# Performance work log

Measured on AMD Instinct MI355X. Metric: run time of the kernel, lower is better.

Reference implementation:

```python
import jax, jax.numpy as jnp
import numpy as np

B, L = 2, 160
RD = 128          # residue_dim
AD = 128          # atom_dim
NUM_AT = 37       # atom37
NSC = 34          # side-chain atom slots (37 - 3 backbone)
EPS = 8.0         # radius for eps_8 graph
NOISE = 0.5       # noise added to repeated CA positions
HID = 512         # decoder MLP hidden


def _precomputed_atom37_mask():
    # Stand-in for VALID_ATOM37_MASK [20 residue types, 37 atoms]:
    # backbone N,CA,C,O always present; deterministic pseudo side-chain counts.
    m = np.zeros((20, NUM_AT), np.float32)
    m[:, :4] = 1.0
    for r in range(20):
        nsc = 1 + (r * 7) % 10
        m[r, 4:4 + nsc] = 1.0
    return jnp.asarray(m)


def setup_inputs() -> dict:
    key = jax.random.key(0)
    ks = jax.random.split(key, 8)
    bb_pred = jax.random.normal(ks[0], (B, L, 3, 3), jnp.float32) * 10.0
    scalar_features = jax.random.normal(ks[1], (B, L, RD), jnp.float32)
    aa_pred = jax.random.normal(ks[2], (B, L, 20), jnp.float32)
    mask = jnp.ones((B, L), jnp.float32)
    residue_batch = jnp.repeat(jnp.arange(B, dtype=jnp.int64), L)
    # learned parameters
    atom_emb = jax.random.normal(ks[3], (NUM_AT, AD), jnp.float32) * 0.02
    W1 = jax.random.normal(ks[4], (2 * AD, HID), jnp.float32) / np.sqrt(2.0 * AD)
    b1 = jnp.zeros((HID,), jnp.float32)
    W2 = jax.random.normal(ks[5], (HID, 3), jnp.float32) / np.sqrt(float(HID))
    b2 = jnp.zeros((3,), jnp.float32)
    # pre-sampled position noise (torch.randn_like * noise)
    pos_noise = jax.random.normal(ks[6], (B, L, NSC, 3), jnp.float32) * NOISE
    precomputed_mask = _precomputed_atom37_mask()
    return dict(bb_pred=bb_pred, scalar_features=scalar_features, aa_pred=aa_pred,
                residue_batch=residue_batch, mask=mask, precomputed_mask=precomputed_mask,
                atom_emb=atom_emb, W1=W1, b1=b1, W2=W2, b2=b2, pos_noise=pos_noise)


def reference(bb_pred, scalar_features, aa_pred, residue_batch, mask,
              precomputed_mask, atom_emb, W1, b1, W2, b2, pos_noise):
    # --- generate_atom37_mask ---
    res_types = jnp.argmax(aa_pred, axis=-1)                       # [B,L]
    atom_mask = precomputed_mask[res_types] * mask[..., None]      # [B,L,37]

    # --- ResidueAndAtomEmbedder (dense, validity carried as mask) ---
    atom_type_emb = atom_emb[None, None] * atom_mask[..., None]    # [B,L,37,AD]
    combined = scalar_features[:, :, None, :] + atom_type_emb      # [B,L,37,AD]
    sc_mask = atom_mask[:, :, 3:]                                  # [B,L,34]
    h = combined[:, :, 3:, :] * sc_mask[..., None]                 # [B,L,34,AD]

    # --- reconstruct_edges: CA repeated per side-chain slot + noise ---
    ca = bb_pred[:, :, 1, :] * mask[..., None]                     # [B,L,3]
    pos = ca[:, :, None, :] + pos_noise                            # [B,L,34,3]

    Ns = L * NSC
    x = pos.reshape(B, Ns, 3)
    hf = h.reshape(B, Ns, AD)
    valid = sc_mask.reshape(B, Ns)                                 # batch axis B == residue_batch separation

    # pairwise squared distances [B,Ns,Ns] (eps_8 radius graph, dense masked form)
    x2 = jnp.sum(x * x, axis=-1)
    d2 = x2[:, :, None] + x2[:, None, :] - 2.0 * jnp.einsum('bnd,bmd->bnm', x, x)
    pair_valid = valid[:, :, None] * valid[:, None, :]
    w = jnp.where(d2 < EPS * EPS, jnp.exp(-d2 / (2.0 * EPS * EPS)), 0.0) * pair_valid

    # --- PositionDecoder (EGNN-style layer, self-loops contribute zero rel-pos) ---
    deg = jnp.sum(w, axis=-1, keepdims=True)                       # [B,Ns,1]
    inv = 1.0 / (deg + 1.0)
    agg_pos = (x * deg - jnp.einsum('bnm,bmd->bnd', w, x)) * inv   # sum_j w_ij (x_i - x_j), normalized
    h_agg = jnp.einsum('bnm,bmd->bnd', w, hf) * inv                # [B,Ns,AD]
    z = jnp.concatenate([hf, h_agg], axis=-1)                      # [B,Ns,2*AD]
    gate = jnp.tanh(jax.nn.relu(z @ W1 + b1) @ W2 + b2)            # [B,Ns,3]
    disp = agg_pos * gate * valid[..., None]

    updated_pos = (x + disp).reshape(B, L, NSC, 3)
    return atom_mask, updated_pos
```

## Files before the change

### kernel.cpp

```cpp
#include <hip/hip_runtime.h>
#include <hip/hip_bf16.h>
#include <math.h>

#define BB 2
#define LL 160
#define NSC 34
#define NS (LL * NSC)
#define TOT (BB * NS)
#define AD 128
#define ADX 144
#define HID 512
#define NAT 37
#define KC 8
#define NVP 1792
#define NVT 28
#define NVPT (BB * NVP)
#define PEN 1.0e9f

typedef __attribute__((ext_vector_type(4))) float f32x4;
typedef __attribute__((ext_vector_type(8))) short s16x8;
typedef __attribute__((address_space(1))) const unsigned int gu32;
typedef __attribute__((address_space(3))) unsigned int lu32;

struct LdsW { float t[64][65]; };
struct LdsPC {
  int sincl[256];
  int smap[NVP];
  short srt[LL];
  float smk[LL];
  float4 sxc[64];
  __hip_bfloat16 tile[ADX][64];
};

__global__ __launch_bounds__(256) void k_prep(
    const float* __restrict__ W1, const float* __restrict__ bb,
    const float* __restrict__ aa, const float* __restrict__ mask,
    const float* __restrict__ pm, const float* __restrict__ noise,
    const float* __restrict__ sf, const float* __restrict__ emb,
    float* __restrict__ out_mask, float* __restrict__ out_pos,
    __hip_bfloat16* __restrict__ W1T, float* __restrict__ ws_val,
    int* __restrict__ cg2g, float4* __restrict__ xc,
    __hip_bfloat16* __restrict__ hfTc, __hip_bfloat16* __restrict__ ws_z,
    int* __restrict__ ws_nv) {
  __shared__ union { LdsW w; LdsPC c; } u;
  int blk = blockIdx.x;
  int tid = threadIdx.x;

  if (blk < 32) {
    int j0 = (blk >> 2) * 64;
    int c0 = (blk & 3) * 64;
    for (int i = tid; i < 64 * 64; i += 256) {
      int jl = i & 63, cl = i >> 6;
      u.w.t[cl][jl] = W1[(size_t)(c0 + cl) * HID + j0 + jl];
    }
    __syncthreads();
    for (int i = tid; i < 64 * 64; i += 256) {
      int cl = i & 63, jl = i >> 6;
      W1T[(size_t)(j0 + jl) * 256 + c0 + cl] = __float2bfloat16(u.w.t[cl][jl]);
    }
    return;
  }

  if (blk < 32 + BB * LL) {
    int bl = blk - 32;
    int b = bl / LL, l = bl % LL;
    const float* ap = aa + bl * 20;
    float mv = ap[0]; int rt = 0;
    for (int r = 1; r < 20; ++r) { float v = ap[r]; if (v > mv) { mv = v; rt = r; } }
    float mk = mask[bl];
    const float* pmr = pm + rt * NAT;
    if (tid < NAT) out_mask[bl * NAT + tid] = pmr[tid] * mk;
    if (tid < NSC) ws_val[b * NS + l * NSC + tid] = pmr[3 + tid] * mk;
    float ca0 = bb[(bl * 3 + 1) * 3 + 0] * mk;
    float ca1 = bb[(bl * 3 + 1) * 3 + 1] * mk;
    float ca2 = bb[(bl * 3 + 1) * 3 + 2] * mk;
    if (tid < NSC * 3) {
      int s = tid / 3, c = tid % 3;
      float ca = (c == 0) ? ca0 : (c == 1) ? ca1 : ca2;
      out_pos[(size_t)(b * NS + l * NSC + s) * 3 + c] = ca + noise[(bl * NSC + s) * 3 + c];
    }
    return;
  }

  int pb = blk - (32 + BB * LL);
  int b = pb / NVT;
  int j0 = (pb % NVT) * 64;

  int c = 0;
  if (tid < LL) {
    int bl = b * LL + tid;
    const float* ap = aa + bl * 20;
    float mv = ap[0]; int rt = 0;
    for (int r = 1; r < 20; ++r) { float v = ap[r]; if (v > mv) { mv = v; rt = r; } }
    float mk = mask[bl];
    u.c.srt[tid] = (short)rt;
    u.c.smk[tid] = mk;
    const float* pmr = pm + rt * NAT + 3;
    for (int s = 0; s < NSC; ++s)
      if (pmr[s] * mk > 0.f) ++c;
  }
  u.c.sincl[tid] = c;
  __syncthreads();
  #pragma unroll
  for (int off = 1; off < 256; off <<= 1) {
    int t = (tid >= off) ? u.c.sincl[tid - off] : 0;
    __syncthreads();
    u.c.sincl[tid] += t;
    __syncthreads();
  }
  if (tid == 0 && j0 == 0) ws_nv[b] = u.c.sincl[LL - 1];
  for (int j = tid; j < NVP; j += 256) u.c.smap[j] = -1;
  __syncthreads();
  if (tid < LL) {
    int o = u.c.sincl[tid] - c, k = 0;
    const float* pmr = pm + (int)u.c.srt[tid] * NAT + 3;
    float mk = u.c.smk[tid];
    for (int s = 0; s < NSC; ++s) {
      if (pmr[s] * mk > 0.f) { u.c.smap[o + k] = tid * NSC + s; ++k; }
    }
  }
  __syncthreads();

  if (tid < 64) {
    int j = j0 + tid;
    int m = u.c.smap[j];
    cg2g[b * NVP + j] = m;
    float4 v;
    if (m >= 0) {
      int l = m / NSC, s = m - l * NSC;
      float mk = u.c.smk[l];
      int bl = b * LL + l;
      const float* npz = noise + (bl * NSC + s) * 3;
      float x = bb[(bl * 3 + 1) * 3 + 0] * mk + npz[0];
      float y = bb[(bl * 3 + 1) * 3 + 1] * mk + npz[1];
      float z = bb[(bl * 3 + 1) * 3 + 2] * mk + npz[2];
      v.x = x; v.y = y; v.z = z;
      v.w = x * x + y * y + z * z;
    } else {
      v.x = 0.f; v.y = 0.f; v.z = 0.f; v.w = PEN;
    }
    xc[b * NVP + j] = v;
    u.c.sxc[tid] = v;
  }
  __syncthreads();

  int jl = tid >> 2, cq = tid & 3;
  int m = u.c.smap[j0 + jl];
  union { s16x8 v[4]; __hip_bfloat16 h[32]; } o;
  if (m >= 0) {
    int l = m / NSC, s = m - l * NSC;
    float am = pm[(int)u.c.srt[l] * NAT + 3 + s] * u.c.smk[l];
    const float* sfp = sf + (size_t)(b * LL + l) * AD + cq * 32;
    const float* emp = emb + (size_t)(3 + s) * AD + cq * 32;
    #pragma unroll 8
    for (int k = 0; k < 32; ++k) {
      float hv = (sfp[k] + emp[k] * am) * am;
      o.h[k] = __float2bfloat16(hv);
      u.c.tile[cq * 32 + k][jl] = o.h[k];
    }
  } else {
    __hip_bfloat16 zz = __float2bfloat16(0.0f);
    #pragma unroll 8
    for (int k = 0; k < 32; ++k) { o.h[k] = zz; u.c.tile[cq * 32 + k][jl] = zz; }
  }
  {
    __hip_bfloat16* zp = ws_z + ((size_t)(b * NVP + j0 + jl)) * 128 + cq * 32;
    #pragma unroll
    for (int q = 0; q < 4; ++q) *(s16x8*)(zp + q * 8) = o.v[q];
  }
  if (cq == 0) {
    float4 xj = u.c.sxc[jl];
    u.c.tile[128][jl] = __float2bfloat16(m >= 0 ? 1.0f : 0.0f);
    u.c.tile[129][jl] = __float2bfloat16(m >= 0 ? xj.x : 0.f);
    u.c.tile[130][jl] = __float2bfloat16(m >= 0 ? xj.y : 0.f);
    u.c.tile[131][jl] = __float2bfloat16(m >= 0 ? xj.z : 0.f);
    __hip_bfloat16 zz = __float2bfloat16(0.0f);
    for (int rr = 132; rr < ADX; ++rr) u.c.tile[rr][jl] = zz;
  }
  __syncthreads();
  for (int i = tid; i < ADX * 2; i += 256) {
    int r = i >> 1, hf = i & 1;
    __hip_bfloat16* dst = hfTc + (size_t)b * ADX * NVP + (size_t)r * NVP + j0 + hf * 32;
    const __hip_bfloat16* srow = &u.c.tile[r][hf * 32];
    #pragma unroll
    for (int q = 0; q < 4; ++q)
      *(s16x8*)(dst + q * 8) = *(const s16x8*)(srow + q * 8);
  }
}

__global__ __launch_bounds__(256, 4) void k_haggc(
    const float4* __restrict__ xc, const __hip_bfloat16* __restrict__ hfTc,
    __hip_bfloat16* __restrict__ haggp, float* __restrict__ dgp,
    const int* __restrict__ ws_nv) {
  constexpr int NSTEP = NVP / 32;
  constexpr int CH_MAX = (NSTEP + KC - 1) / KC;
  __shared__ float4 xs[(CH_MAX * 4 + 1) * 9];
  __shared__ alignas(16) __hip_bfloat16 sB[2][4608];

  int bid = blockIdx.x;
  int b = bid / (NVT * KC);
  int rem = bid % (NVT * KC);
  int kc = rem / NVT;
  int nt = rem % NVT;
  int n0 = nt * 64;
  int nv = ws_nv[b];
  if (n0 >= nv) return;
  int sb = (kc * NSTEP) / KC, se = ((kc + 1) * NSTEP) / KC;
  int nstep_eff = (nv + 31) >> 5;
  int se2 = se < nstep_eff ? se : nstep_eff;
  int tid = threadIdx.x, w = tid >> 6, lane = tid & 63;
  int ln = lane & 15, g8 = (lane >> 4) * 8;

  const float4* xb = xc + b * NVP;
  const __hip_bfloat16* hb = hfTc + (size_t)b * ADX * NVP;

  float4 xn = xb[n0 + w * 16 + ln];
  float x2n = xn.w;

  f32x4 acc[9];
  #pragma unroll
  for (int ct = 0; ct < 9; ++ct) acc[ct] = (f32x4){0.f, 0.f, 0.f, 0.f};

  auto STAGE = [&](int s, int pb) {
    const char* srcb = (const char*)(hb + (size_t)s * 32);
    #pragma unroll
    for (int k = 0; k < 3; ++k) {
      int t = tid + k * 256;
      if (t < 576) {
        int row = t >> 2;
        int sl = (t & 3) ^ (row & 3);
        const gu32* gp = (const gu32*)(const void*)(srcb + (size_t)row * (NVP * 2) + sl * 16);
        lu32* lp = (lu32*)(void*)((char*)&sB[pb][0] + (size_t)(t & ~63) * 16);
        __builtin_amdgcn_global_load_lds(gp, lp, 16, 0, 0);
      }
    }
  };

  if (sb < se2) {
    int mcnt = (se2 - sb) * 32;
    for (int i = tid; i < mcnt; i += 256)
      xs[(i >> 3) * 9 + (i & 7)] = xb[sb * 32 + i];

    STAGE(sb, 0);
    __syncthreads();

    int cur = 0;
    for (int s = sb; s < se2; ++s) {
      if (s + 1 < se2) STAGE(s + 1, cur ^ 1);
      int grp = (s - sb) * 4 + (g8 >> 3);
      union { s16x8 v; __hip_bfloat16 h[8]; } af;
      #pragma unroll
      for (int j = 0; j < 8; ++j) {
        float4 xm = xs[grp * 9 + j];
        float dt = xn.x * xm.x + xn.y * xm.y + xn.z * xm.z;
        float d2 = x2n + xm.w - 2.f * dt;
        float wv = (d2 < 64.f) ? __expf(d2 * -0.0078125f) : 0.f;
        af.h[j] = __float2bfloat16(wv);
      }
      const char* bbase = (const char*)&sB[cur][0];
      int slot = g8 >> 3;
      #pragma unroll
      for (int ct = 0; ct < 9; ++ct) {
        int row = ct * 16 + ln;
        int boff = (row << 6) + ((slot ^ (row & 3)) << 4);
        s16x8 bf = *(const s16x8*)(bbase + boff);
        acc[ct] = __builtin_amdgcn_mfma_f32_16x16x32_bf16(af.v, bf, acc[ct], 0, 0, 0);
      }
      __syncthreads();
      cur ^= 1;
    }
  }

  int q = lane >> 4;
  int grow = b * NVP + n0 + w * 16 + q * 4;
  #pragma unroll
  for (int ct = 0; ct < 8; ++ct)
    #pragma unroll
    for (int r = 0; r < 4; ++r)
      haggp[((size_t)kc * NVPT + grow + r) * AD + ct * 16 + ln] = __float2bfloat16(acc[ct][r]);
  if (ln < 4)
    #pragma unroll
    for (int r = 0; r < 4; ++r)
      dgp[((size_t)kc * NVPT + grow + r) * 4 + ln] = acc[8][r];
}

__global__ __launch_bounds__(512) void k_mlpf(
    const __hip_bfloat16* __restrict__ ws_z,
    const __hip_bfloat16* __restrict__ haggp, const float* __restrict__ dgp,
    const __hip_bfloat16* __restrict__ W1T, const float* __restrict__ b1v,
    const float* __restrict__ W2, const float* __restrict__ b2v,
    const float4* __restrict__ xc, const int* __restrict__ cg2g,
    const float* __restrict__ ws_val, float* __restrict__ out_pos,
    const int* __restrict__ ws_nv) {
  __shared__ __hip_bfloat16 zt[32][136];
  __shared__ float sai[32][4];
  __shared__ float ppart[4][32][3];

  int r0 = blockIdx.x * 32;
  int bq0 = r0 / NVP;
  if (r0 - bq0 * NVP >= ws_nv[bq0]) return;

  int tid = threadIdx.x, w = tid >> 6, lane = tid & 63;
  int ln = lane & 15, g8 = (lane >> 4) * 8, q = lane >> 4;
  int rowhalf = w & 1, js4 = w >> 1;

  if (tid < 32) {
    int g = r0 + tid;
    float deg = 0.f, wx = 0.f, wy = 0.f, wz = 0.f;
    #pragma unroll
    for (int kc = 0; kc < KC; ++kc) {
      float4 d = *(const float4*)&dgp[((size_t)kc * NVPT + g) * 4];
      deg += d.x; wx += d.y; wy += d.z; wz += d.w;
    }
    float inv = 1.f / (deg + 1.f);
    float4 xv = xc[g];
    sai[tid][0] = (xv.x * deg - wx) * inv;
    sai[tid][1] = (xv.y * deg - wy) * inv;
    sai[tid][2] = (xv.z * deg - wz) * inv;
    sai[tid][3] = inv;
  }
  __syncthreads();
  {
    int row = tid >> 4, c8 = tid & 15;
    int g = r0 + row;
    float s[8];
    #pragma unroll
    for (int j = 0; j < 8; ++j) s[j] = 0.f;
    #pragma unroll
    for (int kc = 0; kc < KC; ++kc) {
      union { s16x8 v; __hip_bfloat16 h[8]; } uu;
      uu.v = *(const s16x8*)(haggp + ((size_t)kc * NVPT + g) * AD + c8 * 8);
      #pragma unroll
      for (int j = 0; j < 8; ++j) s[j] += __bfloat162float(uu.h[j]);
    }
    float inv = sai[row][3];
    #pragma unroll
    for (int j = 0; j < 8; ++j)
      zt[row][c8 * 8 + j] = __float2bfloat16(s[j] * inv);
  }
  __syncthreads();

  int arl = rowhalf * 16 + ln;
  int arow = r0 + arl;
  s16x8 a[8];
  #pragma unroll
  for (int kq = 0; kq < 4; ++kq)
    a[kq] = *(const s16x8*)(ws_z + (size_t)arow * 128 + kq * 32 + g8);
  #pragma unroll
  for (int kq = 4; kq < 8; ++kq)
    a[kq] = *(const s16x8*)&zt[arl][(kq - 4) * 32 + g8];

  float p[4][3];
  #pragma unroll
  for (int r = 0; r < 4; ++r)
    #pragma unroll
    for (int o = 0; o < 3; ++o) p[r][o] = 0.f;

  #pragma unroll
  for (int jt = 0; jt < 8; ++jt) {
    int j = js4 * 128 + jt * 16 + ln;
    f32x4 acc = (f32x4){0.f, 0.f, 0.f, 0.f};
    #pragma unroll
    for (int kq = 0; kq < 8; ++kq) {
      s16x8 bw = *(const s16x8*)(W1T + (size_t)j * 256 + kq * 32 + g8);
      acc = __builtin_amdgcn_mfma_f32_16x16x32_bf16(a[kq], bw, acc, 0, 0, 0);
    }
    float bias = b1v[j];
    float w20 = W2[j * 3 + 0], w21 = W2[j * 3 + 1], w22 = W2[j * 3 + 2];
    #pragma unroll
    for (int r = 0; r < 4; ++r) {
      float h = fmaxf(acc[r] + bias, 0.f);
      p[r][0] += h * w20; p[r][1] += h * w21; p[r][2] += h * w22;
    }
  }
  #pragma unroll
  for (int r = 0; r < 4; ++r)
    #pragma unroll
    for (int o = 0; o < 3; ++o) {
      p[r][o] += __shfl_xor(p[r][o], 1);
      p[r][o] += __shfl_xor(p[r][o], 2);
      p[r][o] += __shfl_xor(p[r][o], 4);
      p[r][o] += __shfl_xor(p[r][o], 8);
    }
  if (ln == 0) {
    #pragma unroll
    for (int r = 0; r < 4; ++r) {
      int row = rowhalf * 16 + q * 4 + r;
      #pragma unroll
      for (int o = 0; o < 3; ++o) ppart[js4][row][o] = p[r][o];
    }
  }
  __syncthreads();

  if (tid < 32) {
    int row = tid;
    int g = r0 + row;
    int bq = g / NVP;
    int m = cg2g[g];
    if (m >= 0) {
      float p0 = b2v[0] + ppart[0][row][0] + ppart[1][row][0] + ppart[2][row][0] + ppart[3][row][0];
      float p1 = b2v[1] + ppart[0][row][1] + ppart[1][row][1] + ppart[2][row][1] + ppart[3][row][1];
      float p2 = b2v[2] + ppart[0][row][2] + ppart[1][row][2] + ppart[2][row][2] + ppart[3][row][2];
      float val = ws_val[bq * NS + m];
      float4 xv = xc[g];
      float* op = out_pos + (size_t)(bq * NS + m) * 3;
      op[0] = xv.x + sai[row][0] * tanhf(p0) * val;
      op[1] = xv.y + sai[row][1] * tanhf(p1) * val;
      op[2] = xv.z + sai[row][2] * tanhf(p2) * val;
    }
  }
}

extern "C" void kernel_launch(void* const* d_in, const int* in_sizes, int n_in,
                              void* d_out, int out_size, void* d_ws, size_t ws_size,
                              hipStream_t stream) {
  const float* bb    = (const float*)d_in[0];
  const float* sf    = (const float*)d_in[1];
  const float* aa    = (const float*)d_in[2];
  const float* mask  = (const float*)d_in[4];
  const float* pm    = (const float*)d_in[5];
  const float* emb   = (const float*)d_in[6];
  const float* W1    = (const float*)d_in[7];
  const float* b1v   = (const float*)d_in[8];
  const float* W2    = (const float*)d_in[9];
  const float* b2v   = (const float*)d_in[10];
  const float* noise = (const float*)d_in[11];

  float* out_mask = (float*)d_out;
  float* out_pos  = (float*)d_out + BB * LL * NAT;

  char* cur = (char*)d_ws;
  auto alloc = [&](size_t bytes) -> char* {
    char* p = cur;
    cur += (bytes + 255) & ~(size_t)255;
    return p;
  };
  int*    ws_nv  = (int*)alloc((size_t)BB * 4);
  float*  ws_val = (float*)alloc((size_t)TOT * 4);
  int*    cg2g   = (int*)alloc((size_t)BB * NVP * 4);
  float4* xc     = (float4*)alloc((size_t)BB * NVP * 16);
  float*  ws_dgp = (float*)alloc((size_t)KC * NVPT * 16);
  __hip_bfloat16* ws_w1t = (__hip_bfloat16*)alloc((size_t)HID * 256 * 2);
  __hip_bfloat16* hfTc   = (__hip_bfloat16*)alloc((size_t)BB * ADX * NVP * 2);
  __hip_bfloat16* haggp  = (__hip_bfloat16*)alloc((size_t)KC * NVPT * AD * 2);
  __hip_bfloat16* ws_z   = (__hip_bfloat16*)alloc((size_t)NVPT * 128 * 2);

  hipLaunchKernelGGL(k_prep, dim3(32 + BB * LL + BB * NVT), dim3(256), 0, stream,
                     W1, bb, aa, mask, pm, noise, sf, emb,
                     out_mask, out_pos, ws_w1t, ws_val, cg2g, xc, hfTc, ws_z, ws_nv);
  hipLaunchKernelGGL(k_haggc, dim3(BB * NVT * KC), dim3(256), 0, stream,
                     xc, hfTc, haggp, ws_dgp, ws_nv);
  hipLaunchKernelGGL(k_mlpf, dim3(NVPT / 32), dim3(512), 0, stream,
                     ws_z, haggp, ws_dgp, ws_w1t, b1v, W2, b2v,
                     xc, cg2g, ws_val, out_pos, ws_nv);
}
```

Measured before the change: 47.26 us.

## Fuse MLP decoder into aggregation kernel via last-block atomic counter

Removes the separate k_mlpf launch. The per-row-tile reduction and gated MLP now run inside k_haggc, executed by whichever K-chunk block finishes last for a tile, detected through a per-tile atomic counter that k_prep zeroes. This saves a kernel launch and the gap between the second and third kernels. In exchange, the MLP tail runs on fewer blocks with 4 waves instead of 8, each wave looping over all 512 hidden columns, so the tail work is less parallel. The fused kernel also needs threadfences and a shared-memory union.

```diff
diff --git a/kernel.cpp b/kernel.cpp
--- a/kernel.cpp
+++ b/kernel.cpp
@@ -41,12 +41,13 @@
     __hip_bfloat16* __restrict__ W1T, float* __restrict__ ws_val,
     int* __restrict__ cg2g, float4* __restrict__ xc,
     __hip_bfloat16* __restrict__ hfTc, __hip_bfloat16* __restrict__ ws_z,
-    int* __restrict__ ws_nv) {
+    int* __restrict__ ws_nv, int* __restrict__ cnt) {
   __shared__ union { LdsW w; LdsPC c; } u;
   int blk = blockIdx.x;
   int tid = threadIdx.x;
 
   if (blk < 32) {
+    if (blk == 0 && tid < BB * NVT) cnt[tid] = 0;
     int j0 = (blk >> 2) * 64;
     int c0 = (blk & 3) * 64;
     for (int i = tid; i < 64 * 64; i += 256) {
@@ -188,14 +189,20 @@
   }
 }
 
+struct LdsHA { float4 xs[29 * 9]; __hip_bfloat16 sB[2][4608]; };
+struct LdsTL { __hip_bfloat16 zt[64][136]; float sai[64][4]; };
+
 __global__ __launch_bounds__(256, 4) void k_haggc(
     const float4* __restrict__ xc, const __hip_bfloat16* __restrict__ hfTc,
     __hip_bfloat16* __restrict__ haggp, float* __restrict__ dgp,
-    const int* __restrict__ ws_nv) {
+    const int* __restrict__ ws_nv, const __hip_bfloat16* __restrict__ ws_z,
+    const __hip_bfloat16* __restrict__ W1T, const float* __restrict__ b1v,
+    const float* __restrict__ W2, const float* __restrict__ b2v,
+    const int* __restrict__ cg2g, const float* __restrict__ ws_val,
+    float* __restrict__ out_pos, int* __restrict__ cnt) {
   constexpr int NSTEP = NVP / 32;
-  constexpr int CH_MAX = (NSTEP + KC - 1) / KC;
-  __shared__ float4 xs[(CH_MAX * 4 + 1) * 9];
-  __shared__ alignas(16) __hip_bfloat16 sB[2][4608];
+  __shared__ union { LdsHA a; LdsTL t; } u;
+  __shared__ int slast;
 
   int bid = blockIdx.x;
   int b = bid / (NVT * KC);
@@ -230,7 +237,7 @@
         int row = t >> 2;
         int sl = (t & 3) ^ (row & 3);
         const gu32* gp = (const gu32*)(const void*)(srcb + (size_t)row * (NVP * 2) + sl * 16);
-        lu32* lp = (lu32*)(void*)((char*)&sB[pb][0] + (size_t)(t & ~63) * 16);
+        lu32* lp = (lu32*)(void*)((char*)&u.a.sB[pb][0] + (size_t)(t & ~63) * 16);
         __builtin_amdgcn_global_load_lds(gp, lp, 16, 0, 0);
       }
     }
@@ -239,7 +246,7 @@
   if (sb < se2) {
     int mcnt = (se2 - sb) * 32;
     for (int i = tid; i < mcnt; i += 256)
-      xs[(i >> 3) * 9 + (i & 7)] = xb[sb * 32 + i];
+      u.a.xs[(i >> 3) * 9 + (i & 7)] = xb[sb * 32 + i];
 
     STAGE(sb, 0);
     __syncthreads();
@@ -251,13 +258,13 @@
       union { s16x8 v; __hip_bfloat16 h[8]; } af;
       #pragma unroll
       for (int j = 0; j < 8; ++j) {
-        float4 xm = xs[grp * 9 + j];
+        float4 xm = u.a.xs[grp * 9 + j];
         float dt = xn.x * xm.x + xn.y * xm.y + xn.z * xm.z;
         float d2 = x2n + xm.w - 2.f * dt;
         float wv = (d2 < 64.f) ? __expf(d2 * -0.0078125f) : 0.f;
         af.h[j] = __float2bfloat16(wv);
       }
-      const char* bbase = (const char*)&sB[cur][0];
+      const char* bbase = (const char*)&u.a.sB[cur][0];
       int slot = g8 >> 3;
       #pragma unroll
       for (int ct = 0; ct < 9; ++ct) {
@@ -272,7 +279,8 @@
   }
 
   int q = lane >> 4;
-  int grow = b * NVP + n0 + w * 16 + q * 4;
+  int grow0 = b * NVP + n0;
+  int grow = grow0 + w * 16 + q * 4;
   #pragma unroll
   for (int ct = 0; ct < 8; ++ct)
     #pragma unroll
@@ -282,73 +290,60 @@
     #pragma unroll
     for (int r = 0; r < 4; ++r)
       dgp[((size_t)kc * NVPT + grow + r) * 4 + ln] = acc[8][r];
-}
-
-__global__ __launch_bounds__(512) void k_mlpf(
-    const __hip_bfloat16* __restrict__ ws_z,
-    const __hip_bfloat16* __restrict__ haggp, const float* __restrict__ dgp,
-    const __hip_bfloat16* __restrict__ W1T, const float* __restrict__ b1v,
-    const float* __restrict__ W2, const float* __restrict__ b2v,
-    const float4* __restrict__ xc, const int* __restrict__ cg2g,
-    const float* __restrict__ ws_val, float* __restrict__ out_pos,
-    const int* __restrict__ ws_nv) {
-  __shared__ __hip_bfloat16 zt[32][136];
-  __shared__ float sai[32][4];
-  __shared__ float ppart[4][32][3];
-
-  int r0 = blockIdx.x * 32;
-  int bq0 = r0 / NVP;
-  if (r0 - bq0 * NVP >= ws_nv[bq0]) return;
-
-  int tid = threadIdx.x, w = tid >> 6, lane = tid & 63;
-  int ln = lane & 15, g8 = (lane >> 4) * 8, q = lane >> 4;
-  int rowhalf = w & 1, js4 = w >> 1;
-
-  if (tid < 32) {
-    int g = r0 + tid;
+
+  __threadfence();
+  __syncthreads();
+  if (tid == 0)
+    slast = (atomicAdd(&cnt[b * NVT + nt], 1) == KC - 1) ? 1 : 0;
+  __syncthreads();
+  if (!slast) return;
+  __threadfence();
+
+  if (tid < 64) {
+    int g = grow0 + tid;
     float deg = 0.f, wx = 0.f, wy = 0.f, wz = 0.f;
     #pragma unroll
-    for (int kc = 0; kc < KC; ++kc) {
-      float4 d = *(const float4*)&dgp[((size_t)kc * NVPT + g) * 4];
+    for (int k2 = 0; k2 < KC; ++k2) {
+      float4 d = *(const float4*)&dgp[((size_t)k2 * NVPT + g) * 4];
       deg += d.x; wx += d.y; wy += d.z; wz += d.w;
     }
     float inv = 1.f / (deg + 1.f);
     float4 xv = xc[g];
-    sai[tid][0] = (xv.x * deg - wx) * inv;
-    sai[tid][1] = (xv.y * deg - wy) * inv;
-    sai[tid][2] = (xv.z * deg - wz) * inv;
-    sai[tid][3] = inv;
-  }
-  __syncthreads();
-  {
-    int row = tid >> 4, c8 = tid & 15;
-    int g = r0 + row;
+    u.t.sai[tid][0] = (xv.x * deg - wx) * inv;
+    u.t.sai[tid][1] = (xv.y * deg - wy) * inv;
+    u.t.sai[tid][2] = (xv.z * deg - wz) * inv;
+    u.t.sai[tid][3] = inv;
+  }
+  __syncthreads();
+  for (int u2 = tid; u2 < 64 * 16; u2 += 256) {
+    int row = u2 >> 4, c8 = u2 & 15;
+    int g = grow0 + row;
     float s[8];
     #pragma unroll
     for (int j = 0; j < 8; ++j) s[j] = 0.f;
     #pragma unroll
-    for (int kc = 0; kc < KC; ++kc) {
+    for (int k2 = 0; k2 < KC; ++k2) {
       union { s16x8 v; __hip_bfloat16 h[8]; } uu;
-      uu.v = *(const s16x8*)(haggp + ((size_t)kc * NVPT + g) * AD + c8 * 8);
+      uu.v = *(const s16x8*)(haggp + ((size_t)k2 * NVPT + g) * AD + c8 * 8);
       #pragma unroll
       for (int j = 0; j < 8; ++j) s[j] += __bfloat162float(uu.h[j]);
     }
-    float inv = sai[row][3];
+    float inv = u.t.sai[row][3];
     #pragma unroll
     for (int j = 0; j < 8; ++j)
-      zt[row][c8 * 8 + j] = __float2bfloat16(s[j] * inv);
-  }
-  __syncthreads();
-
-  int arl = rowhalf * 16 + ln;
-  int arow = r0 + arl;
+      u.t.zt[row][c8 * 8 + j] = __float2bfloat16(s[j] * inv);
+  }
+  __syncthreads();
+
+  int arl = w * 16 + ln;
+  int arow = grow0 + arl;
   s16x8 a[8];
   #pragma unroll
   for (int kq = 0; kq < 4; ++kq)
     a[kq] = *(const s16x8*)(ws_z + (size_t)arow * 128 + kq * 32 + g8);
   #pragma unroll
   for (int kq = 4; kq < 8; ++kq)
-    a[kq] = *(const s16x8*)&zt[arl][(kq - 4) * 32 + g8];
+    a[kq] = *(const s16x8*)&u.t.zt[arl][(kq - 4) * 32 + g8];
 
   float p[4][3];
   #pragma unroll
@@ -356,20 +351,19 @@
     #pragma unroll
     for (int o = 0; o < 3; ++o) p[r][o] = 0.f;
 
-  #pragma unroll
-  for (int jt = 0; jt < 8; ++jt) {
-    int j = js4 * 128 + jt * 16 + ln;
-    f32x4 acc = (f32x4){0.f, 0.f, 0.f, 0.f};
+  for (int jt = 0; jt < 32; ++jt) {
+    int j = jt * 16 + ln;
+    f32x4 ac2 = (f32x4){0.f, 0.f, 0.f, 0.f};
     #pragma unroll
     for (int kq = 0; kq < 8; ++kq) {
       s16x8 bw = *(const s16x8*)(W1T + (size_t)j * 256 + kq * 32 + g8);
-      acc = __builtin_amdgcn_mfma_f32_16x16x32_bf16(a[kq], bw, acc, 0, 0, 0);
+      ac2 = __builtin_amdgcn_mfma_f32_16x16x32_bf16(a[kq], bw, ac2, 0, 0, 0);
     }
     float bias = b1v[j];
     float w20 = W2[j * 3 + 0], w21 = W2[j * 3 + 1], w22 = W2[j * 3 + 2];
     #pragma unroll
     for (int r = 0; r < 4; ++r) {
-      float h = fmaxf(acc[r] + bias, 0.f);
+      float h = fmaxf(ac2[r] + bias, 0.f);
       p[r][0] += h * w20; p[r][1] += h * w21; p[r][2] += h * w22;
     }
   }
@@ -385,28 +379,17 @@
   if (ln == 0) {
     #pragma unroll
     for (int r = 0; r < 4; ++r) {
-      int row = rowhalf * 16 + q * 4 + r;
-      #pragma unroll
-      for (int o = 0; o < 3; ++o) ppart[js4][row][o] = p[r][o];
-    }
-  }
-  __syncthreads();
-
-  if (tid < 32) {
-    int row = tid;
-    int g = r0 + row;
-    int bq = g / NVP;
-    int m = cg2g[g];
-    if (m >= 0) {
-      float p0 = b2v[0] + ppart[0][row][0] + ppart[1][row][0] + ppart[2][row][0] + ppart[3][row][0];
-      float p1 = b2v[1] + ppart[0][row][1] + ppart[1][row][1] + ppart[2][row][1] + ppart[3][row][1];
-      float p2 = b2v[2] + ppart[0][row][2] + ppart[1][row][2] + ppart[2][row][2] + ppart[3][row][2];
-      float val = ws_val[bq * NS + m];
-      float4 xv = xc[g];
-      float* op = out_pos + (size_t)(bq * NS + m) * 3;
-      op[0] = xv.x + sai[row][0] * tanhf(p0) * val;
-      op[1] = xv.y + sai[row][1] * tanhf(p1) * val;
-      op[2] = xv.z + sai[row][2] * tanhf(p2) * val;
+      int row = w * 16 + q * 4 + r;
+      int g = grow0 + row;
+      int m = cg2g[g];
+      if (m >= 0) {
+        float val = ws_val[b * NS + m];
+        float4 xv = xc[g];
+        float* op = out_pos + (size_t)(b * NS + m) * 3;
+        op[0] = xv.x + u.t.sai[row][0] * tanhf(p[r][0] + b2v[0]) * val;
+        op[1] = xv.y + u.t.sai[row][1] * tanhf(p[r][1] + b2v[1]) * val;
+        op[2] = xv.z + u.t.sai[row][2] * tanhf(p[r][2] + b2v[2]) * val;
+      }
     }
   }
 }
@@ -436,6 +419,7 @@
     return p;
   };
   int*    ws_nv  = (int*)alloc((size_t)BB * 4);
+  int*    cnt    = (int*)alloc((size_t)BB * NVT * 4);
   float*  ws_val = (float*)alloc((size_t)TOT * 4);
   int*    cg2g   = (int*)alloc((size_t)BB * NVP * 4);
   float4* xc     = (float4*)alloc((size_t)BB * NVP * 16);
@@ -447,10 +431,9 @@
 
   hipLaunchKernelGGL(k_prep, dim3(32 + BB * LL + BB * NVT), dim3(256), 0, stream,
                      W1, bb, aa, mask, pm, noise, sf, emb,
-                     out_mask, out_pos, ws_w1t, ws_val, cg2g, xc, hfTc, ws_z, ws_nv);
+                     out_mask, out_pos, ws_w1t, ws_val, cg2g, xc, hfTc, ws_z,
+                     ws_nv, cnt);
   hipLaunchKernelGGL(k_haggc, dim3(BB * NVT * KC), dim3(256), 0, stream,
-                     xc, hfTc, haggp, ws_dgp, ws_nv);
-  hipLaunchKernelGGL(k_mlpf, dim3(NVPT / 32), dim3(512), 0, stream,
-                     ws_z, haggp, ws_dgp, ws_w1t, b1v, W2, b2v,
-                     xc, cg2g, ws_val, out_pos, ws_nv);
+                     xc, hfTc, haggp, ws_dgp, ws_nv, ws_z,
+                     ws_w1t, b1v, W2, b2v, cg2g, ws_val, out_pos, cnt);
 }
```

After: 131.3 us. 2.78x slower.
